# Kernel tuning notes

Hardware: AMD Instinct MI355X
Metric: run time of the kernel (lower is better)

Reference implementation:

```python
import jax, jax.numpy as jnp
import numpy as np

EPS = 1e-3  # Keras BatchNormalization default epsilon


def _bn(x, gamma, beta, mean, var):
    # inference batch norm, channels-last
    inv = gamma * jax.lax.rsqrt(var + EPS)
    return x * inv + (beta - mean * inv)


def setup_inputs() -> dict:
    key = jax.random.key(0)
    ks = jax.random.split(key, 13)
    B, D, H, W, C, F = 2, 48, 48, 48, 64, 128
    return {
        "x": jax.random.normal(ks[0], (B, D, H, W, C), dtype=jnp.float32),
        "dw_kernel": jax.random.normal(ks[1], (3, 3, 3, 1, C), dtype=jnp.float32) * 0.1,
        "dw_bias": jax.random.normal(ks[2], (C,), dtype=jnp.float32) * 0.1,
        "bn1_gamma": jax.random.uniform(ks[3], (C,), dtype=jnp.float32, minval=0.5, maxval=1.5),
        "bn1_beta": jax.random.normal(ks[4], (C,), dtype=jnp.float32) * 0.1,
        "bn1_mean": jax.random.normal(ks[5], (C,), dtype=jnp.float32) * 0.1,
        "bn1_var": jax.random.uniform(ks[6], (C,), dtype=jnp.float32, minval=0.5, maxval=1.5),
        "pw_kernel": jax.random.normal(ks[7], (C, F), dtype=jnp.float32) * 0.1,
        "pw_bias": jax.random.normal(ks[8], (F,), dtype=jnp.float32) * 0.1,
        "bn2_gamma": jax.random.uniform(ks[9], (F,), dtype=jnp.float32, minval=0.5, maxval=1.5),
        "bn2_beta": jax.random.normal(ks[10], (F,), dtype=jnp.float32) * 0.1,
        "bn2_mean": jax.random.normal(ks[11], (F,), dtype=jnp.float32) * 0.1,
        "bn2_var": jax.random.uniform(ks[12], (F,), dtype=jnp.float32, minval=0.5, maxval=1.5),
    }


def reference(x, dw_kernel, dw_bias, bn1_gamma, bn1_beta, bn1_mean, bn1_var,
              pw_kernel, pw_bias, bn2_gamma, bn2_beta, bn2_mean, bn2_var):
    C = x.shape[-1]
    # True depthwise conv3d (replaces the per-channel Python loop of Conv3D(1,...))
    y = jax.lax.conv_general_dilated(
        x, dw_kernel,
        window_strides=(1, 1, 1), padding="SAME",
        dimension_numbers=("NDHWC", "DHWIO", "NDHWC"),
        feature_group_count=C,
    ) + dw_bias
    y = jax.nn.relu(_bn(y, bn1_gamma, bn1_beta, bn1_mean, bn1_var))
    # pointwise 1x1x1 conv == channel GEMM
    z = jnp.einsum("bdhwc,cf->bdhwf", y, pw_kernel) + pw_bias
    z = jax.nn.relu(_bn(z, bn2_gamma, bn2_beta, bn2_mean, bn2_var))
    return z
```

## Files before the change

### kernel.cpp

```cpp
#include <hip/hip_runtime.h>
#include <hip/hip_bf16.h>

#define EPS 1e-3f

typedef __attribute__((ext_vector_type(8))) short short8;
typedef __attribute__((ext_vector_type(4))) float v4f;

__device__ __forceinline__ unsigned short f2bf(float f) {
    unsigned int u = __float_as_uint(f);
    unsigned int r = (u + 0x7fffu + ((u >> 16) & 1u)) >> 16;
    return (unsigned short)r;
}

__global__ __launch_bounds__(256) void prep_kernel(
    const float* __restrict__ dwb,
    const float* __restrict__ g1, const float* __restrict__ b1,
    const float* __restrict__ m1, const float* __restrict__ v1,
    const float* __restrict__ pw, const float* __restrict__ pwb,
    const float* __restrict__ g2, const float* __restrict__ b2,
    const float* __restrict__ m2, const float* __restrict__ v2,
    float* __restrict__ scale1, float* __restrict__ shift1,
    float* __restrict__ s2, float* __restrict__ t2,
    unsigned short* __restrict__ Wt)
{
    int tid = threadIdx.x;
    if (blockIdx.x == 0) {
        if (tid < 64) {
            float inv = g1[tid] * rsqrtf(v1[tid] + EPS);
            scale1[tid] = inv;
            shift1[tid] = dwb[tid] * inv + b1[tid] - m1[tid] * inv;
        }
        if (tid < 128) {
            float inv = g2[tid] * rsqrtf(v2[tid] + EPS);
            s2[tid] = inv;
            t2[tid] = pwb[tid] * inv + b2[tid] - m2[tid] * inv;
        }
    }
    int idx = blockIdx.x * 256 + tid;
    int j     = idx & 7;
    int lane  = (idx >> 3) & 63;
    int kstep = (idx >> 9) & 1;
    int ntile = idx >> 10;
    int k = kstep * 32 + (lane >> 4) * 8 + j;
    int f = ntile * 16 + (lane & 15);
    Wt[idx] = f2bf(pw[k * 128 + f]);
}

__global__ __launch_bounds__(256, 3) void fused_kernel(
    const float* __restrict__ x,
    const float* __restrict__ wgt,
    const float* __restrict__ scale1,
    const float* __restrict__ shift1,
    const unsigned short* __restrict__ Wt,
    const float* __restrict__ s2,
    const float* __restrict__ t2,
    float* __restrict__ out)
{
    __shared__ float wS[27 * 64];
    __shared__ float sS[64];
    __shared__ float tS[64];
    __shared__ float s2S[128];
    __shared__ float t2S[128];
    __shared__ float xS[6 * 18 * 66];
    __shared__ unsigned short yS[64 * 72];

    int tid = threadIdx.x;
    for (int i = tid; i < 27 * 64; i += 256) wS[i] = wgt[i];
    if (tid < 64) { sS[tid] = scale1[tid]; tS[tid] = shift1[tid]; }
    if (tid < 128) { s2S[tid] = s2[tid]; t2S[tid] = t2[tid]; }
    __syncthreads();

    int n   = blockIdx.x;
    int xcd = n & 7;
    int j   = n >> 3;
    int bdg = xcd * 3 + j / 36;
    int hw  = j % 36;
    int b    = bdg / 12;
    int dgrp = bdg % 12;
    int d0   = dgrp * 4;
    int w0  = (hw % 3) * 16;
    int h0  = (hw / 3) * 4;

    int tx = tid & 15;
    int ty = tid >> 4;
    int c0 = tx * 4;
    int wq = ty & 3;
    int rh = ty >> 2;

    int wv   = tid >> 6;
    int lane = tid & 63;
    int lrow = lane & 15;
    int quad = lane >> 4;

    float4 acc[3][4];
    #pragma unroll
    for (int a = 0; a < 3; ++a)
        #pragma unroll
        for (int r = 0; r < 4; ++r) acc[a][r] = make_float4(0.f, 0.f, 0.f, 0.f);

    #pragma unroll
    for (int k = 0; k < 6; ++k) {
        int s = d0 - 1 + k;
        bool s_ok = (s >= 0) && (s < 48);

        if (s_ok) {
            const float* xs = x + (long)(b * 48 + s) * (48 * 48 * 64);
            #pragma unroll
            for (int i = 0; i < 7; ++i) {
                int idx = i * 256 + tid;
                if (idx < 1728) {
                    int cg = idx & 15;
                    int hwl = idx >> 4;
                    int hh = hwl / 18;
                    int ww = hwl - hh * 18;
                    int zh = h0 + hh - 1;
                    int zw = w0 + ww - 1;
                    float4 v = make_float4(0.f, 0.f, 0.f, 0.f);
                    if (zh >= 0 && zh < 48 && zw >= 0 && zw < 48)
                        v = *(const float4*)(xs + (zh * 48 + zw) * 64 + cg * 4);
                    *(float4*)(&xS[(hh * 18 + ww) * 66 + cg * 4]) = v;
                }
            }
        }
        __syncthreads();

        if (s_ok) {
            #pragma unroll
            for (int hh = 0; hh < 3; ++hh) {
                const float* rp = &xS[((rh + hh) * 18 + wq * 4) * 66 + c0];
                float4 xv[6];
                #pragma unroll
                for (int p = 0; p < 6; ++p)
                    xv[p] = *(const float4*)(rp + p * 66);
                #pragma unroll
                for (int m = 0; m < 4; ++m) {
                    if (m >= k - 2 && m <= k) {
                        const int wz  = k - m;
                        const int aid = m % 3;
                        #pragma unroll
                        for (int ww = 0; ww < 3; ++ww) {
                            const float4 wvv = *(const float4*)(&wS[((wz * 3 + hh) * 3 + ww) * 64 + c0]);
                            #pragma unroll
                            for (int r = 0; r < 4; ++r) {
                                acc[aid][r].x += xv[r + ww].x * wvv.x;
                                acc[aid][r].y += xv[r + ww].y * wvv.y;
                                acc[aid][r].z += xv[r + ww].z * wvv.z;
                                acc[aid][r].w += xv[r + ww].w * wvv.w;
                            }
                        }
                    }
                }
            }
        }

        if (k >= 2) {
            const int m   = k - 2;
            const int aid = m % 3;
            {
                float4 s1 = *(const float4*)(&sS[c0]);
                float4 t1 = *(const float4*)(&tS[c0]);
                #pragma unroll
                for (int r = 0; r < 4; ++r) {
                    ushort4 o;
                    o.x = f2bf(fmaxf(acc[aid][r].x * s1.x + t1.x, 0.f));
                    o.y = f2bf(fmaxf(acc[aid][r].y * s1.y + t1.y, 0.f));
                    o.z = f2bf(fmaxf(acc[aid][r].z * s1.z + t1.z, 0.f));
                    o.w = f2bf(fmaxf(acc[aid][r].w * s1.w + t1.w, 0.f));
                    *(ushort4*)(&yS[(ty * 4 + r) * 72 + c0]) = o;
                    acc[aid][r] = make_float4(0.f, 0.f, 0.f, 0.f);
                }
            }
            __syncthreads();

            const short8 a0 = *(const short8*)(&yS[(wv * 16 + lrow) * 72 + quad * 8]);
            const short8 a1 = *(const short8*)(&yS[(wv * 16 + lrow) * 72 + 32 + quad * 8]);

            v4f g[8];
            #pragma unroll
            for (int nn = 0; nn < 8; ++nn) g[nn] = (v4f){0.f, 0.f, 0.f, 0.f};

            #pragma unroll
            for (int nn = 0; nn < 8; ++nn) {
                short8 b0 = *(const short8*)(Wt + ((nn * 2 + 0) * 64 + lane) * 8);
                short8 b1 = *(const short8*)(Wt + ((nn * 2 + 1) * 64 + lane) * 8);
                g[nn] = __builtin_amdgcn_mfma_f32_16x16x32_bf16(a0, b0, g[nn], 0, 0, 0);
                g[nn] = __builtin_amdgcn_mfma_f32_16x16x32_bf16(a1, b1, g[nn], 0, 0, 0);
            }

            int d = d0 + m;
            long base_out = ((((long)b * 48 + d) * 48 + (h0 + wv)) * 48 + w0) * 128;
            #pragma unroll
            for (int nn = 0; nn < 8; ++nn) {
                int f = nn * 16 + lrow;
                float sf = s2S[f];
                float tf = t2S[f];
                #pragma unroll
                for (int r = 0; r < 4; ++r) {
                    float v = fmaxf(g[nn][r] * sf + tf, 0.f);
                    out[base_out + (quad * 4 + r) * 128 + f] = v;
                }
            }
        } else {
            __syncthreads();
        }
    }
}

extern "C" void kernel_launch(void* const* d_in, const int* in_sizes, int n_in,
                              void* d_out, int out_size, void* d_ws, size_t ws_size,
                              hipStream_t stream)
{
    const float* x   = (const float*)d_in[0];
    const float* dwk = (const float*)d_in[1];
    const float* dwb = (const float*)d_in[2];
    const float* g1  = (const float*)d_in[3];
    const float* b1  = (const float*)d_in[4];
    const float* m1  = (const float*)d_in[5];
    const float* v1  = (const float*)d_in[6];
    const float* pw  = (const float*)d_in[7];
    const float* pwb = (const float*)d_in[8];
    const float* g2  = (const float*)d_in[9];
    const float* b2  = (const float*)d_in[10];
    const float* m2  = (const float*)d_in[11];
    const float* v2  = (const float*)d_in[12];

    float* outp = (float*)d_out;

    float* scale1 = (float*)d_ws;
    float* shift1 = scale1 + 64;
    float* s2     = scale1 + 128;
    float* t2     = scale1 + 256;
    unsigned short* Wt = (unsigned short*)((char*)d_ws + 2048);

    hipLaunchKernelGGL(prep_kernel, dim3(32), dim3(256), 0, stream,
                       dwb, g1, b1, m1, v1, pw, pwb, g2, b2, m2, v2,
                       scale1, shift1, s2, t2, Wt);

    hipLaunchKernelGGL(fused_kernel, dim3(864), dim3(256), 0, stream,
                       x, dwk, scale1, shift1, Wt, s2, t2, outp);
}
```

Before: 235.8 us.

## Prefetch next depth slab into registers and enlarge depth tile to six

```diff
diff --git a/kernel.cpp b/kernel.cpp
--- a/kernel.cpp
+++ b/kernel.cpp
@@ -68,16 +68,15 @@
     for (int i = tid; i < 27 * 64; i += 256) wS[i] = wgt[i];
     if (tid < 64) { sS[tid] = scale1[tid]; tS[tid] = shift1[tid]; }
     if (tid < 128) { s2S[tid] = s2[tid]; t2S[tid] = t2[tid]; }
-    __syncthreads();
 
     int n   = blockIdx.x;
     int xcd = n & 7;
     int j   = n >> 3;
-    int bdg = xcd * 3 + j / 36;
+    int bdg = xcd * 2 + j / 36;
     int hw  = j % 36;
-    int b    = bdg / 12;
-    int dgrp = bdg % 12;
-    int d0   = dgrp * 4;
+    int b    = bdg >> 3;
+    int dgrp = bdg & 7;
+    int d0   = dgrp * 6;
     int w0  = (hw % 3) * 16;
     int h0  = (hw / 3) * 4;
 
@@ -92,6 +91,45 @@
     int lrow = lane & 15;
     int quad = lane >> 4;
 
+    int  g_off[7], l_off[7];
+    bool ldm[7], wrm[7];
+    #pragma unroll
+    for (int i = 0; i < 7; ++i) {
+        int idx = i * 256 + tid;
+        bool active = idx < 1728;
+        int cg  = idx & 15;
+        int hwl = idx >> 4;
+        int hh  = hwl / 18;
+        int ww  = hwl - hh * 18;
+        int zh  = h0 + hh - 1;
+        int zw  = w0 + ww - 1;
+        bool inb = active && zh >= 0 && zh < 48 && zw >= 0 && zw < 48;
+        g_off[i] = (zh * 48 + zw) * 64 + cg * 4;
+        l_off[i] = (hh * 18 + ww) * 66 + cg * 4;
+        ldm[i] = inb;
+        wrm[i] = active;
+    }
+
+    const long slab_stride = 48 * 48 * 64;
+    const float* xbase = x + (long)b * 48 * slab_stride;
+
+    float4 R[7];
+    {
+        int s = d0 - 1;
+        if (s >= 0) {
+            const float* xs = xbase + (long)s * slab_stride;
+            #pragma unroll
+            for (int i = 0; i < 7; ++i)
+                if (ldm[i]) R[i] = *(const float4*)(xs + g_off[i]);
+        }
+    }
+    short8 bf[16];
+    #pragma unroll
+    for (int nn = 0; nn < 16; ++nn)
+        bf[nn] = *(const short8*)(Wt + (nn * 64 + lane) * 8);
+
+    __syncthreads();
+
     float4 acc[3][4];
     #pragma unroll
     for (int a = 0; a < 3; ++a)
@@ -99,29 +137,28 @@
         for (int r = 0; r < 4; ++r) acc[a][r] = make_float4(0.f, 0.f, 0.f, 0.f);
 
     #pragma unroll
-    for (int k = 0; k < 6; ++k) {
+    for (int k = 0; k < 8; ++k) {
         int s = d0 - 1 + k;
         bool s_ok = (s >= 0) && (s < 48);
 
         if (s_ok) {
-            const float* xs = x + (long)(b * 48 + s) * (48 * 48 * 64);
-            #pragma unroll
-            for (int i = 0; i < 7; ++i) {
-                int idx = i * 256 + tid;
-                if (idx < 1728) {
-                    int cg = idx & 15;
-                    int hwl = idx >> 4;
-                    int hh = hwl / 18;
-                    int ww = hwl - hh * 18;
-                    int zh = h0 + hh - 1;
-                    int zw = w0 + ww - 1;
-                    float4 v = make_float4(0.f, 0.f, 0.f, 0.f);
-                    if (zh >= 0 && zh < 48 && zw >= 0 && zw < 48)
-                        v = *(const float4*)(xs + (zh * 48 + zw) * 64 + cg * 4);
-                    *(float4*)(&xS[(hh * 18 + ww) * 66 + cg * 4]) = v;
-                }
-            }
-        }
+            #pragma unroll
+            for (int i = 0; i < 7; ++i)
+                if (wrm[i])
+                    *(float4*)(&xS[l_off[i]]) =
+                        ldm[i] ? R[i] : make_float4(0.f, 0.f, 0.f, 0.f);
+        }
+
+        if (k < 7) {
+            int sn = s + 1;
+            if (sn >= 0 && sn < 48) {
+                const float* xs = xbase + (long)sn * slab_stride;
+                #pragma unroll
+                for (int i = 0; i < 7; ++i)
+                    if (ldm[i]) R[i] = *(const float4*)(xs + g_off[i]);
+            }
+        }
+
         __syncthreads();
 
         if (s_ok) {
@@ -133,7 +170,7 @@
                 for (int p = 0; p < 6; ++p)
                     xv[p] = *(const float4*)(rp + p * 66);
                 #pragma unroll
-                for (int m = 0; m < 4; ++m) {
+                for (int m = 0; m < 6; ++m) {
                     if (m >= k - 2 && m <= k) {
                         const int wz  = k - m;
                         const int aid = m % 3;
@@ -154,24 +191,25 @@
         }
 
         if (k >= 2) {
-            const int m   = k - 2;
-            const int aid = m % 3;
-            {
-                float4 s1 = *(const float4*)(&sS[c0]);
-                float4 t1 = *(const float4*)(&tS[c0]);
-                #pragma unroll
-                for (int r = 0; r < 4; ++r) {
-                    ushort4 o;
-                    o.x = f2bf(fmaxf(acc[aid][r].x * s1.x + t1.x, 0.f));
-                    o.y = f2bf(fmaxf(acc[aid][r].y * s1.y + t1.y, 0.f));
-                    o.z = f2bf(fmaxf(acc[aid][r].z * s1.z + t1.z, 0.f));
-                    o.w = f2bf(fmaxf(acc[aid][r].w * s1.w + t1.w, 0.f));
-                    *(ushort4*)(&yS[(ty * 4 + r) * 72 + c0]) = o;
-                    acc[aid][r] = make_float4(0.f, 0.f, 0.f, 0.f);
-                }
-            }
-            __syncthreads();
-
+            const int aid = (k - 2) % 3;
+            float4 s1 = *(const float4*)(&sS[c0]);
+            float4 t1 = *(const float4*)(&tS[c0]);
+            #pragma unroll
+            for (int r = 0; r < 4; ++r) {
+                ushort4 o;
+                o.x = f2bf(fmaxf(acc[aid][r].x * s1.x + t1.x, 0.f));
+                o.y = f2bf(fmaxf(acc[aid][r].y * s1.y + t1.y, 0.f));
+                o.z = f2bf(fmaxf(acc[aid][r].z * s1.z + t1.z, 0.f));
+                o.w = f2bf(fmaxf(acc[aid][r].w * s1.w + t1.w, 0.f));
+                *(ushort4*)(&yS[(ty * 4 + r) * 72 + c0]) = o;
+                acc[aid][r] = make_float4(0.f, 0.f, 0.f, 0.f);
+            }
+        }
+
+        __syncthreads();
+
+        if (k >= 2) {
+            const int m = k - 2;
             const short8 a0 = *(const short8*)(&yS[(wv * 16 + lrow) * 72 + quad * 8]);
             const short8 a1 = *(const short8*)(&yS[(wv * 16 + lrow) * 72 + 32 + quad * 8]);
 
@@ -181,10 +219,8 @@
 
             #pragma unroll
             for (int nn = 0; nn < 8; ++nn) {
-                short8 b0 = *(const short8*)(Wt + ((nn * 2 + 0) * 64 + lane) * 8);
-                short8 b1 = *(const short8*)(Wt + ((nn * 2 + 1) * 64 + lane) * 8);
-                g[nn] = __builtin_amdgcn_mfma_f32_16x16x32_bf16(a0, b0, g[nn], 0, 0, 0);
-                g[nn] = __builtin_amdgcn_mfma_f32_16x16x32_bf16(a1, b1, g[nn], 0, 0, 0);
+                g[nn] = __builtin_amdgcn_mfma_f32_16x16x32_bf16(a0, bf[nn * 2 + 0], g[nn], 0, 0, 0);
+                g[nn] = __builtin_amdgcn_mfma_f32_16x16x32_bf16(a1, bf[nn * 2 + 1], g[nn], 0, 0, 0);
             }
 
             int d = d0 + m;
@@ -200,8 +236,6 @@
                     out[base_out + (quad * 4 + r) * 128 + f] = v;
                 }
             }
-        } else {
-            __syncthreads();
         }
     }
 }
@@ -236,6 +270,6 @@
                        dwb, g1, b1, m1, v1, pw, pwb, g2, b2, m2, v2,
                        scale1, shift1, s2, t2, Wt);
 
-    hipLaunchKernelGGL(fused_kernel, dim3(864), dim3(256), 0, stream,
+    hipLaunchKernelGGL(fused_kernel, dim3(576), dim3(256), 0, stream,
                        x, dwk, scale1, shift1, Wt, s2, t2, outp);
 }
```

Result: slower. 476.4 us (+102.0%).

## Load depthwise inputs directly from global memory and deepen per-block D tile

Applied to the files above, without the earlier changes.

```diff
diff --git a/kernel.cpp b/kernel.cpp
--- a/kernel.cpp
+++ b/kernel.cpp
@@ -61,7 +61,6 @@
     __shared__ float tS[64];
     __shared__ float s2S[128];
     __shared__ float t2S[128];
-    __shared__ float xS[6 * 18 * 66];
     __shared__ unsigned short yS[64 * 72];
 
     int tid = threadIdx.x;
@@ -71,13 +70,12 @@
     __syncthreads();
 
     int n   = blockIdx.x;
-    int xcd = n & 7;
-    int j   = n >> 3;
-    int bdg = xcd * 3 + j / 36;
-    int hw  = j % 36;
-    int b    = bdg / 12;
-    int dgrp = bdg % 12;
-    int d0   = dgrp * 4;
+    int g   = (n & 7) * 72 + (n >> 3);
+    int bdg = g / 36;
+    int hw  = g % 36;
+    int b    = bdg >> 3;
+    int dgrp = bdg & 7;
+    int d0   = dgrp * 6;
     int w0  = (hw % 3) * 16;
     int h0  = (hw / 3) * 4;
 
@@ -92,6 +90,26 @@
     int lrow = lane & 15;
     int quad = lane >> 4;
 
+    int w0t = w0 + wq * 4;
+    float mwL = (w0t >= 1)  ? 1.f : 0.f;
+    float mwR = (w0t <= 43) ? 1.f : 0.f;
+    int wcl[6];
+    #pragma unroll
+    for (int p = 0; p < 6; ++p)
+        wcl[p] = min(max(w0t - 1 + p, 0), 47) * 64;
+
+    int h = h0 + rh;
+    bool hok[3];
+    int  hcl[3];
+    #pragma unroll
+    for (int hh = 0; hh < 3; ++hh) {
+        int zh = h + hh - 1;
+        hok[hh] = (zh >= 0 && zh < 48);
+        hcl[hh] = min(max(zh, 0), 47) * 48 * 64;
+    }
+
+    const long slab_stride = 48 * 48 * 64;
+
     float4 acc[3][4];
     #pragma unroll
     for (int a = 0; a < 3; ++a)
@@ -99,53 +117,37 @@
         for (int r = 0; r < 4; ++r) acc[a][r] = make_float4(0.f, 0.f, 0.f, 0.f);
 
     #pragma unroll
-    for (int k = 0; k < 6; ++k) {
+    for (int k = 0; k < 8; ++k) {
         int s = d0 - 1 + k;
         bool s_ok = (s >= 0) && (s < 48);
 
         if (s_ok) {
-            const float* xs = x + (long)(b * 48 + s) * (48 * 48 * 64);
-            #pragma unroll
-            for (int i = 0; i < 7; ++i) {
-                int idx = i * 256 + tid;
-                if (idx < 1728) {
-                    int cg = idx & 15;
-                    int hwl = idx >> 4;
-                    int hh = hwl / 18;
-                    int ww = hwl - hh * 18;
-                    int zh = h0 + hh - 1;
-                    int zw = w0 + ww - 1;
-                    float4 v = make_float4(0.f, 0.f, 0.f, 0.f);
-                    if (zh >= 0 && zh < 48 && zw >= 0 && zw < 48)
-                        v = *(const float4*)(xs + (zh * 48 + zw) * 64 + cg * 4);
-                    *(float4*)(&xS[(hh * 18 + ww) * 66 + cg * 4]) = v;
-                }
-            }
-        }
-        __syncthreads();
-
-        if (s_ok) {
+            const float* dp = x + ((long)(b * 48 + s) * 48 * 48) * 64 + c0;
             #pragma unroll
             for (int hh = 0; hh < 3; ++hh) {
-                const float* rp = &xS[((rh + hh) * 18 + wq * 4) * 66 + c0];
-                float4 xv[6];
-                #pragma unroll
-                for (int p = 0; p < 6; ++p)
-                    xv[p] = *(const float4*)(rp + p * 66);
-                #pragma unroll
-                for (int m = 0; m < 4; ++m) {
-                    if (m >= k - 2 && m <= k) {
-                        const int wz  = k - m;
-                        const int aid = m % 3;
-                        #pragma unroll
-                        for (int ww = 0; ww < 3; ++ww) {
-                            const float4 wvv = *(const float4*)(&wS[((wz * 3 + hh) * 3 + ww) * 64 + c0]);
+                if (hok[hh]) {
+                    const float* rowp = dp + hcl[hh];
+                    float4 xv[6];
+                    #pragma unroll
+                    for (int p = 0; p < 6; ++p)
+                        xv[p] = *(const float4*)(rowp + wcl[p]);
+                    xv[0].x *= mwL; xv[0].y *= mwL; xv[0].z *= mwL; xv[0].w *= mwL;
+                    xv[5].x *= mwR; xv[5].y *= mwR; xv[5].z *= mwR; xv[5].w *= mwR;
+                    #pragma unroll
+                    for (int m = 0; m < 6; ++m) {
+                        if (m >= k - 2 && m <= k) {
+                            const int wz  = k - m;
+                            const int aid = m % 3;
                             #pragma unroll
-                            for (int r = 0; r < 4; ++r) {
-                                acc[aid][r].x += xv[r + ww].x * wvv.x;
-                                acc[aid][r].y += xv[r + ww].y * wvv.y;
-                                acc[aid][r].z += xv[r + ww].z * wvv.z;
-                                acc[aid][r].w += xv[r + ww].w * wvv.w;
+                            for (int ww = 0; ww < 3; ++ww) {
+                                const float4 wvv = *(const float4*)(&wS[((wz * 3 + hh) * 3 + ww) * 64 + c0]);
+                                #pragma unroll
+                                for (int r = 0; r < 4; ++r) {
+                                    acc[aid][r].x += xv[r + ww].x * wvv.x;
+                                    acc[aid][r].y += xv[r + ww].y * wvv.y;
+                                    acc[aid][r].z += xv[r + ww].z * wvv.z;
+                                    acc[aid][r].w += xv[r + ww].w * wvv.w;
+                                }
                             }
                         }
                     }
@@ -156,6 +158,9 @@
         if (k >= 2) {
             const int m   = k - 2;
             const int aid = m % 3;
+
+            __syncthreads();
+
             {
                 float4 s1 = *(const float4*)(&sS[c0]);
                 float4 t1 = *(const float4*)(&tS[c0]);
@@ -175,16 +180,16 @@
             const short8 a0 = *(const short8*)(&yS[(wv * 16 + lrow) * 72 + quad * 8]);
             const short8 a1 = *(const short8*)(&yS[(wv * 16 + lrow) * 72 + 32 + quad * 8]);
 
-            v4f g[8];
-            #pragma unroll
-            for (int nn = 0; nn < 8; ++nn) g[nn] = (v4f){0.f, 0.f, 0.f, 0.f};
+            v4f gacc[8];
+            #pragma unroll
+            for (int nn = 0; nn < 8; ++nn) gacc[nn] = (v4f){0.f, 0.f, 0.f, 0.f};
 
             #pragma unroll
             for (int nn = 0; nn < 8; ++nn) {
                 short8 b0 = *(const short8*)(Wt + ((nn * 2 + 0) * 64 + lane) * 8);
                 short8 b1 = *(const short8*)(Wt + ((nn * 2 + 1) * 64 + lane) * 8);
-                g[nn] = __builtin_amdgcn_mfma_f32_16x16x32_bf16(a0, b0, g[nn], 0, 0, 0);
-                g[nn] = __builtin_amdgcn_mfma_f32_16x16x32_bf16(a1, b1, g[nn], 0, 0, 0);
+                gacc[nn] = __builtin_amdgcn_mfma_f32_16x16x32_bf16(a0, b0, gacc[nn], 0, 0, 0);
+                gacc[nn] = __builtin_amdgcn_mfma_f32_16x16x32_bf16(a1, b1, gacc[nn], 0, 0, 0);
             }
 
             int d = d0 + m;
@@ -196,12 +201,10 @@
                 float tf = t2S[f];
                 #pragma unroll
                 for (int r = 0; r < 4; ++r) {
-                    float v = fmaxf(g[nn][r] * sf + tf, 0.f);
+                    float v = fmaxf(gacc[nn][r] * sf + tf, 0.f);
                     out[base_out + (quad * 4 + r) * 128 + f] = v;
                 }
             }
-        } else {
-            __syncthreads();
         }
     }
 }
@@ -236,6 +239,6 @@
                        dwb, g1, b1, m1, v1, pw, pwb, g2, b2, m2, v2,
                        scale1, shift1, s2, t2, Wt);
 
-    hipLaunchKernelGGL(fused_kernel, dim3(864), dim3(256), 0, stream,
+    hipLaunchKernelGGL(fused_kernel, dim3(576), dim3(256), 0, stream,
                        x, dwk, scale1, shift1, Wt, s2, t2, outp);
 }
```

Result: faster. 205.5 us (-12.9%).
